# Performance work log

Hardware: AMD Instinct MI355X
Metric: run time of the kernel (lower is better)

Reference implementation:

```python
import jax, jax.numpy as jnp
import numpy as np

N, D, T = 4096, 256, 8
RHO = 16.0
DT = 1.0 / T


def setup_inputs() -> dict:
    key = jax.random.key(0)
    k1, k2, k3, k4 = jax.random.split(key, 4)
    X = jax.random.normal(k1, (N, D), dtype=jnp.float32)
    # learned deformation parameters (small init so the Euler flow stays stable)
    A = jax.random.normal(k2, (T, N, D), dtype=jnp.float32) * 0.01
    A_aff = jax.random.normal(k3, (T, D, D), dtype=jnp.float32) * 0.01
    b_aff = jax.random.normal(k4, (T, D), dtype=jnp.float32) * 0.01
    return {"X": X, "A": A, "A_aff": A_aff, "b_aff": b_aff}


def _flow(X, A, A_aff, b_aff):
    inv_two_rho2 = 1.0 / (2.0 * RHO * RHO)

    def step(Z, params_t):
        A_t, Aaff_t, baff_t = params_t
        # Gaussian self-kernel K[i,j] = exp(-||z_i - z_j||^2 / (2 rho^2))
        sq = jnp.sum(Z * Z, axis=1)                      # [n]
        dist = sq[:, None] + sq[None, :] - 2.0 * (Z @ Z.T)  # [n, n]
        K = jnp.exp(-dist * inv_two_rho2)
        # velocity: affine part + RKHS (kernel message aggregation) part
        v = Z @ Aaff_t.T + baff_t[None, :] + K @ A_t     # [n, d]
        return Z + DT * v, None

    Z_final, _ = jax.lax.scan(step, X, (A, A_aff, b_aff))
    return Z_final


def reference(X, A, A_aff, b_aff):
    return _flow(X, A, A_aff, b_aff)
```

## Files before the change

kernel.cpp:

```cpp
#include <hip/hip_runtime.h>


#define N_PTS 4096
#define DIM   256
#define DT_C  0.125f
#define C1    (1.0f/512.0f)

typedef __bf16 bf16x8 __attribute__((ext_vector_type(8)));
typedef float  f32x16 __attribute__((ext_vector_type(16)));
typedef float  f32x4v __attribute__((ext_vector_type(4)));
typedef unsigned int   u32x4 __attribute__((ext_vector_type(4)));
typedef unsigned short u16x8 __attribute__((ext_vector_type(8)));

__device__ __forceinline__ unsigned short f2bf(float f) {
  unsigned int u = __builtin_bit_cast(unsigned int, f);
  u += 0x7fffu + ((u >> 16) & 1u);
  return (unsigned short)(u >> 16);
}
__device__ __forceinline__ float bf2f(unsigned short s) {
  unsigned int u = ((unsigned int)s) << 16;
  return __builtin_bit_cast(float, u);
}

__global__ __launch_bounds__(256) void k_prep(const float* __restrict__ A,
                                              unsigned short* __restrict__ ATf) {
  __shared__ float sT[64][36];
  const int jgrp = blockIdx.x, ds = blockIdx.y, t = blockIdx.z;
  const int tid = threadIdx.x;
  const float* Ab = A + (size_t)t * N_PTS * DIM;
  {
    const int j_l = tid >> 2, dq = tid & 3;
    const float* src = Ab + (size_t)(jgrp * 64 + j_l) * DIM + ds * 32 + dq * 8;
    f32x4v v0 = *(const f32x4v*)src, v1 = *(const f32x4v*)(src + 4);
    *(f32x4v*)&sT[j_l][dq * 8] = v0;
    *(f32x4v*)&sT[j_l][dq * 8 + 4] = v1;
  }
  __syncthreads();
  const int jb_l = tid >> 6, l = tid & 63, l31 = l & 31, lhi = l >> 5;
  u16x8 o;
#pragma unroll
  for (int e = 0; e < 8; ++e) o[e] = f2bf(sT[jb_l * 16 + lhi * 8 + e][l31]);
  unsigned short* dst = ATf + (size_t)t * (8 * 256 * 64 * 8)
                      + ((size_t)(ds * 256 + jgrp * 4 + jb_l) * 64 + l) * 8;
  *(u16x8*)dst = o;
}

__global__ __launch_bounds__(256) void k_init(const float* __restrict__ X,
                                              unsigned short* __restrict__ Zf,
                                              float* __restrict__ erow) {
  const int tid = threadIdx.x;
  const int r = blockIdx.x * 8 + (tid >> 5), o = tid & 31;
  const size_t base = (size_t)r * DIM + o * 8;
  f32x4v z0 = *(const f32x4v*)(X + base), z1 = *(const f32x4v*)(X + base + 4);
  u16x8 zb; float s = 0.f;
#pragma unroll
  for (int i = 0; i < 4; ++i) { zb[i] = f2bf(z0[i]); zb[4 + i] = f2bf(z1[i]);
                                s += z0[i] * z0[i] + z1[i] * z1[i]; }
  *(u16x8*)(Zf + ((size_t)((r >> 5) * 16 + (o >> 1)) * 64 + (o & 1) * 32 + (r & 31)) * 8) = zb;
#pragma unroll
  for (int d = 16; d > 0; d >>= 1) s += __shfl_down(s, d, 32);
  if (o == 0) erow[r] = __expf(-s * C1);
}

__global__ __launch_bounds__(512, 4) void k_flash(
    const unsigned short* __restrict__ Zf, const float* __restrict__ erow,
    const unsigned short* __restrict__ ATf_t,
    const float* __restrict__ Aaff_t,
    unsigned short* __restrict__ Opart) {
  __shared__ unsigned short sP[2][64 * 64];

  const int tid = threadIdx.x, lane = tid & 63, wid = tid >> 6;
  const int l31 = lane & 31, lhi = lane >> 5;
  const int chunk = blockIdx.x;
  const int i0 = blockIdx.y * 64;
  const int ib = i0 >> 5;

  if (wid < 4) {
    const int ip = wid >> 1, jh = wid & 1;
    bf16x8 af[16];
    {
      const unsigned short* ap = Zf + ((size_t)(ib + ip) * 16 * 64 + lane) * 8;
#pragma unroll
      for (int ks = 0; ks < 16; ++ks)
        af[ks] = __builtin_bit_cast(bf16x8, *(const u32x4*)(ap + ks * 512));
    }
    float eI[16];
#pragma unroll
    for (int c = 0; c < 16; ++c)
      eI[c] = erow[i0 + ip * 32 + 4 * lhi + (c & 3) + 8 * (c >> 2)];

    for (int n = 0; n < 8; ++n) {
      f32x16 S;
#pragma unroll
      for (int i = 0; i < 16; ++i) S[i] = 0.f;
      {
        const int jblk = chunk * 16 + n * 2 + jh;
        const unsigned short* bp = Zf + ((size_t)jblk * 16 * 64 + lane) * 8;
#pragma unroll
        for (int ks = 0; ks < 16; ++ks) {
          bf16x8 b = __builtin_bit_cast(bf16x8, *(const u32x4*)(bp + ks * 512));
          S = __builtin_amdgcn_mfma_f32_32x32x16_bf16(af[ks], b, S, 0, 0, 0);
        }
      }
      const float ej = erow[chunk * 512 + n * 64 + jh * 32 + l31];
      unsigned short* pb = sP[n & 1];
      const int blk = jh * 4 + (l31 >> 3), cl = l31 & 7;
#pragma unroll
      for (int c = 0; c < 16; ++c) {
        const int row = ip * 32 + 4 * lhi + (c & 3) + 8 * (c >> 2);
        pb[row * 64 + ((blk ^ (row & 7)) * 8) + cl] =
            f2bf(eI[c] * ej * __expf(2.f * C1 * S[c]));
      }
      __syncthreads();
    }
    __syncthreads();
  } else {
    const int cd = wid - 4;
    f32x16 O[2][2];
#pragma unroll
    for (int rs = 0; rs < 2; ++rs)
#pragma unroll
      for (int ct = 0; ct < 2; ++ct)
#pragma unroll
        for (int i = 0; i < 16; ++i) O[rs][ct][i] = 0.f;

#pragma unroll
    for (int q = 0; q < 2; ++q) {
      const int ksg = chunk * 2 + q;
      bf16x8 a[2];
#pragma unroll
      for (int rs = 0; rs < 2; ++rs)
        a[rs] = __builtin_bit_cast(bf16x8, *(const u32x4*)(
            Zf + (((size_t)(ib + rs) * 16 + ksg) * 64 + lane) * 8));
#pragma unroll
      for (int ct = 0; ct < 2; ++ct) {
        const int d = cd * 64 + ct * 32 + l31;
        const float* bp = Aaff_t + (size_t)d * DIM + ksg * 16 + lhi * 8;
        f32x4v f0 = *(const f32x4v*)bp, f1 = *(const f32x4v*)(bp + 4);
        u16x8 tb;
#pragma unroll
        for (int i = 0; i < 4; ++i) { tb[i] = f2bf(f0[i]); tb[4 + i] = f2bf(f1[i]); }
        bf16x8 bv = __builtin_bit_cast(bf16x8, tb);
#pragma unroll
        for (int rs = 0; rs < 2; ++rs)
          O[rs][ct] = __builtin_amdgcn_mfma_f32_32x32x16_bf16(a[rs], bv, O[rs][ct], 0, 0, 0);
      }
    }
    __syncthreads();

    for (int n = 1; n <= 8; ++n) {
      const int m = n - 1;
      const unsigned short* pb = sP[m & 1];
#pragma unroll
      for (int ks = 0; ks < 4; ++ks) {
        bf16x8 a[2], b[2];
        const int blk = ks * 2 + lhi;
#pragma unroll
        for (int rs = 0; rs < 2; ++rs) {
          const int row = rs * 32 + l31;
          a[rs] = *(const bf16x8*)&pb[row * 64 + ((blk ^ (row & 7)) * 8)];
        }
#pragma unroll
        for (int ct = 0; ct < 2; ++ct)
          b[ct] = __builtin_bit_cast(bf16x8, *(const u32x4*)(ATf_t +
              ((size_t)((cd * 2 + ct) * 256 + chunk * 32 + m * 4 + ks) * 64 + lane) * 8));
#pragma unroll
        for (int rs = 0; rs < 2; ++rs)
#pragma unroll
          for (int ct = 0; ct < 2; ++ct)
            O[rs][ct] = __builtin_amdgcn_mfma_f32_32x32x16_bf16(a[rs], b[ct], O[rs][ct], 0, 0, 0);
      }
      __syncthreads();
    }

    unsigned short* ob = Opart + (size_t)chunk * N_PTS * DIM + (size_t)cd * 64 + l31;
#pragma unroll
    for (int rs = 0; rs < 2; ++rs)
#pragma unroll
      for (int c = 0; c < 16; ++c) {
        const int row = i0 + rs * 32 + 4 * lhi + (c & 3) + 8 * (c >> 2);
        ob[(size_t)row * DIM]      = f2bf(O[rs][0][c]);
        ob[(size_t)row * DIM + 32] = f2bf(O[rs][1][c]);
      }
  }
}

__global__ __launch_bounds__(256) void k_update(const float* __restrict__ Zin,
                                                const unsigned short* __restrict__ Opart,
                                                const float* __restrict__ baff_t,
                                                float* __restrict__ Zout,
                                                unsigned short* __restrict__ Zf,
                                                float* __restrict__ erow) {
  const int tid = threadIdx.x;
  const int r = blockIdx.x * 8 + (tid >> 5), o = tid & 31;
  const size_t base = (size_t)r * DIM + o * 8;
  f32x4v z0 = *(const f32x4v*)(Zin + base), z1 = *(const f32x4v*)(Zin + base + 4);
  f32x4v s0 = *(const f32x4v*)(baff_t + o * 8), s1 = *(const f32x4v*)(baff_t + o * 8 + 4);
#pragma unroll
  for (int c = 0; c < 8; ++c) {
    u16x8 p = *(const u16x8*)(Opart + (size_t)c * N_PTS * DIM + base);
#pragma unroll
    for (int i = 0; i < 4; ++i) { s0[i] += bf2f(p[i]); s1[i] += bf2f(p[4 + i]); }
  }
  u16x8 zb; float sv = 0.f;
#pragma unroll
  for (int i = 0; i < 4; ++i) {
    z0[i] += DT_C * s0[i]; z1[i] += DT_C * s1[i];
    zb[i] = f2bf(z0[i]); zb[4 + i] = f2bf(z1[i]);
    sv += z0[i] * z0[i] + z1[i] * z1[i];
  }
  *(f32x4v*)(Zout + base) = z0;
  *(f32x4v*)(Zout + base + 4) = z1;
  *(u16x8*)(Zf + ((size_t)((r >> 5) * 16 + (o >> 1)) * 64 + (o & 1) * 32 + (r & 31)) * 8) = zb;
#pragma unroll
  for (int d = 16; d > 0; d >>= 1) sv += __shfl_down(sv, d, 32);
  if (o == 0) erow[r] = __expf(-sv * C1);
}

extern "C" void kernel_launch(void* const* d_in, const int* in_sizes, int n_in,
                              void* d_out, int out_size, void* d_ws, size_t ws_size,
                              hipStream_t stream) {
  const float* X    = (const float*)d_in[0];
  const float* A    = (const float*)d_in[1];
  const float* Aaff = (const float*)d_in[2];
  const float* baff = (const float*)d_in[3];
  float* out = (float*)d_out;

  char* w = (char*)d_ws;
  size_t off = 0;
  unsigned short* ATf = (unsigned short*)(w + off); off += (size_t)8 * 8 * 256 * 64 * 8 * 2;
  unsigned short* Zf  = (unsigned short*)(w + off); off += (size_t)N_PTS * DIM * 2;
  float* erow = (float*)(w + off); off += (size_t)N_PTS * 4;
  float* Zf32 = (float*)(w + off); off += (size_t)N_PTS * DIM * 4;
  unsigned short* Opart = (unsigned short*)(w + off); off += (size_t)8 * N_PTS * DIM * 2;
  (void)ws_size; (void)in_sizes; (void)n_in; (void)out_size;

  k_prep<<<dim3(64, 8, 8), 256, 0, stream>>>(A, ATf);
  k_init<<<512, 256, 0, stream>>>(X, Zf, erow);

  const float* zin = X;
  for (int t = 0; t < 8; ++t) {
    float* zout = (t == 7) ? out : Zf32;
    k_flash<<<dim3(8, 64), 512, 0, stream>>>(
        Zf, erow, ATf + (size_t)t * (8 * 256 * 64 * 8), Aaff + (size_t)t * DIM * DIM, Opart);
    k_update<<<512, 256, 0, stream>>>(zin, Opart, baff + (size_t)t * DIM, zout, Zf, erow);
    zin = zout;
  }
}
```

Measured before the change: 391.3 us.

## Fuse score and aggregation per wave, keeping kernel tile in registers

Replaces the producer/consumer warp split in k_flash (4 waves computing exp scores into shared memory, 4 waves consuming them) with 4 waves that each compute scores via transposed MFMA and feed them directly as the B operand of the K@A MFMA, using lane shuffles instead of LDS and __syncthreads. Block size drops to 256 threads, register-prefetched Z_j and A tiles overlap with the math, and output is staged through a per-wave LDS bounce buffer for coalesced 16-byte stores. Each wave now recomputes its own score tile for its half of D, which doubles the score MFMA work, and register pressure rises.

```diff
diff --git a/kernel.cpp b/kernel.cpp
--- a/kernel.cpp
+++ b/kernel.cpp
@@ -20,6 +20,10 @@
 __device__ __forceinline__ float bf2f(unsigned short s) {
   unsigned int u = ((unsigned int)s) << 16;
   return __builtin_bit_cast(float, u);
+}
+__device__ __forceinline__ unsigned int packtr(float lo, float hi) {
+  return __builtin_amdgcn_perm(__builtin_bit_cast(unsigned int, hi),
+                               __builtin_bit_cast(unsigned int, lo), 0x07060302u);
 }
 
 __global__ __launch_bounds__(256) void k_prep(const float* __restrict__ A,
@@ -62,126 +66,157 @@
   if (o == 0) erow[r] = __expf(-s * C1);
 }
 
-__global__ __launch_bounds__(512, 4) void k_flash(
+__global__ __launch_bounds__(256, 2) void k_flash(
     const unsigned short* __restrict__ Zf, const float* __restrict__ erow,
     const unsigned short* __restrict__ ATf_t,
     const float* __restrict__ Aaff_t,
     unsigned short* __restrict__ Opart) {
-  __shared__ unsigned short sP[2][64 * 64];
+  __shared__ __align__(16) unsigned short bounce[4][32 * 136];
 
   const int tid = threadIdx.x, lane = tid & 63, wid = tid >> 6;
   const int l31 = lane & 31, lhi = lane >> 5;
+  const int isub = wid & 1, dh = wid >> 1;
   const int chunk = blockIdx.x;
   const int i0 = blockIdx.y * 64;
-  const int ib = i0 >> 5;
-
-  if (wid < 4) {
-    const int ip = wid >> 1, jh = wid & 1;
-    bf16x8 af[16];
+
+  bf16x8 zi[16];
+  {
+    const unsigned short* zp = Zf + ((size_t)(blockIdx.y * 2 + isub) * 16 * 64 + lane) * 8;
+#pragma unroll
+    for (int ks = 0; ks < 16; ++ks)
+      zi[ks] = __builtin_bit_cast(bf16x8, *(const u32x4*)(zp + ks * 512));
+  }
+  const float ei = erow[i0 + isub * 32 + l31];
+
+  f32x16 Op[4];
+#pragma unroll
+  for (int d = 0; d < 4; ++d)
+#pragma unroll
+    for (int i = 0; i < 16; ++i) Op[d][i] = 0.f;
+
+#pragma unroll
+  for (int q = 0; q < 2; ++q) {
+    const int ksg = chunk * 2 + q;
+    bf16x8 bzi = zi[ksg];
+#pragma unroll
+    for (int dblk = 0; dblk < 4; ++dblk) {
+      const int d = dh * 128 + dblk * 32 + l31;
+      const float* ap = Aaff_t + (size_t)d * DIM + ksg * 16 + lhi * 8;
+      f32x4v f0 = *(const f32x4v*)ap, f1 = *(const f32x4v*)(ap + 4);
+      u16x8 tb;
+#pragma unroll
+      for (int i = 0; i < 4; ++i) { tb[i] = f2bf(f0[i]); tb[4 + i] = f2bf(f1[i]); }
+      Op[dblk] = __builtin_amdgcn_mfma_f32_32x32x16_bf16(
+          __builtin_bit_cast(bf16x8, tb), bzi, Op[dblk], 0, 0, 0);
+    }
+  }
+
+  const unsigned short* zjbase = Zf + ((size_t)(chunk * 16) * 16 * 64 + lane) * 8;
+  const unsigned short* atbase = ATf_t + ((size_t)(dh * 4 * 256 + chunk * 32) * 64 + lane) * 8;
+  const float* ejbase = erow + chunk * 512 + 4 * lhi;
+
+  u32x4 zj[8], at[8];
+  u32x4 B0 = {0, 0, 0, 0}, B1 = {0, 0, 0, 0};
+#pragma unroll
+  for (int k = 0; k < 8; ++k) zj[k] = *(const u32x4*)(zjbase + (size_t)k * 512);
+
+#pragma unroll 1
+  for (int n = 0; n < 16; ++n) {
+    if (n) {
+      bf16x8 bb0 = __builtin_bit_cast(bf16x8, B0);
+      bf16x8 bb1 = __builtin_bit_cast(bf16x8, B1);
+#pragma unroll
+      for (int dblk = 0; dblk < 4; ++dblk)
+        Op[dblk] = __builtin_amdgcn_mfma_f32_32x32x16_bf16(
+            __builtin_bit_cast(bf16x8, at[dblk * 2]), bb0, Op[dblk], 0, 0, 0);
+#pragma unroll
+      for (int dblk = 0; dblk < 4; ++dblk)
+        Op[dblk] = __builtin_amdgcn_mfma_f32_32x32x16_bf16(
+            __builtin_bit_cast(bf16x8, at[dblk * 2 + 1]), bb1, Op[dblk], 0, 0, 0);
+    }
+#pragma unroll
+    for (int dblk = 0; dblk < 4; ++dblk)
+#pragma unroll
+      for (int s = 0; s < 2; ++s)
+        at[dblk * 2 + s] = *(const u32x4*)(atbase +
+            ((size_t)dblk * 256 + n * 2 + s) * 512);
+
+    f32x16 Sa, Sb;
+#pragma unroll
+    for (int i = 0; i < 16; ++i) { Sa[i] = 0.f; Sb[i] = 0.f; }
     {
-      const unsigned short* ap = Zf + ((size_t)(ib + ip) * 16 * 64 + lane) * 8;
-#pragma unroll
-      for (int ks = 0; ks < 16; ++ks)
-        af[ks] = __builtin_bit_cast(bf16x8, *(const u32x4*)(ap + ks * 512));
-    }
-    float eI[16];
-#pragma unroll
-    for (int c = 0; c < 16; ++c)
-      eI[c] = erow[i0 + ip * 32 + 4 * lhi + (c & 3) + 8 * (c >> 2)];
-
-    for (int n = 0; n < 8; ++n) {
-      f32x16 S;
-#pragma unroll
-      for (int i = 0; i < 16; ++i) S[i] = 0.f;
-      {
-        const int jblk = chunk * 16 + n * 2 + jh;
-        const unsigned short* bp = Zf + ((size_t)jblk * 16 * 64 + lane) * 8;
-#pragma unroll
-        for (int ks = 0; ks < 16; ++ks) {
-          bf16x8 b = __builtin_bit_cast(bf16x8, *(const u32x4*)(bp + ks * 512));
-          S = __builtin_amdgcn_mfma_f32_32x32x16_bf16(af[ks], b, S, 0, 0, 0);
+      const unsigned short* zt = zjbase + (size_t)n * 8192;
+#pragma unroll
+      for (int k = 0; k < 8; ++k)
+        Sa = __builtin_amdgcn_mfma_f32_32x32x16_bf16(
+            __builtin_bit_cast(bf16x8, zj[k]), zi[k], Sa, 0, 0, 0);
+#pragma unroll
+      for (int k = 0; k < 8; ++k) zj[k] = *(const u32x4*)(zt + (size_t)(8 + k) * 512);
+#pragma unroll
+      for (int k = 0; k < 8; ++k)
+        Sb = __builtin_amdgcn_mfma_f32_32x32x16_bf16(
+            __builtin_bit_cast(bf16x8, zj[k]), zi[k + 8], Sb, 0, 0, 0);
+      if (n < 15) {
+#pragma unroll
+        for (int k = 0; k < 8; ++k)
+          zj[k] = *(const u32x4*)(zt + (size_t)(16 + k) * 512);
+      }
+    }
+    {
+      unsigned int G[8];
+#pragma unroll
+      for (int g = 0; g < 4; ++g) {
+        f32x4v ejv = *(const f32x4v*)(ejbase + n * 32 + 8 * g);
+#pragma unroll
+        for (int p = 0; p < 2; ++p) {
+          const int c = g * 4 + p * 2;
+          float p0 = ei * ejv[p * 2]     * __expf(2.f * C1 * (Sa[c] + Sb[c]));
+          float p1 = ei * ejv[p * 2 + 1] * __expf(2.f * C1 * (Sa[c + 1] + Sb[c + 1]));
+          G[g * 2 + p] = packtr(p0, p1);
         }
       }
-      const float ej = erow[chunk * 512 + n * 64 + jh * 32 + l31];
-      unsigned short* pb = sP[n & 1];
-      const int blk = jh * 4 + (l31 >> 3), cl = l31 & 7;
-#pragma unroll
-      for (int c = 0; c < 16; ++c) {
-        const int row = ip * 32 + 4 * lhi + (c & 3) + 8 * (c >> 2);
-        pb[row * 64 + ((blk ^ (row & 7)) * 8) + cl] =
-            f2bf(eI[c] * ej * __expf(2.f * C1 * S[c]));
+      unsigned int Gp[8];
+#pragma unroll
+      for (int r = 0; r < 8; ++r) Gp[r] = __shfl_xor((int)G[r], 32);
+      B0[0] = lhi ? Gp[2] : G[0];  B0[1] = lhi ? Gp[3] : G[1];
+      B0[2] = lhi ? G[2] : Gp[0];  B0[3] = lhi ? G[3] : Gp[1];
+      B1[0] = lhi ? Gp[6] : G[4];  B1[1] = lhi ? Gp[7] : G[5];
+      B1[2] = lhi ? G[6] : Gp[4];  B1[3] = lhi ? G[7] : Gp[5];
+    }
+  }
+  {
+    bf16x8 bb0 = __builtin_bit_cast(bf16x8, B0);
+    bf16x8 bb1 = __builtin_bit_cast(bf16x8, B1);
+#pragma unroll
+    for (int dblk = 0; dblk < 4; ++dblk)
+      Op[dblk] = __builtin_amdgcn_mfma_f32_32x32x16_bf16(
+          __builtin_bit_cast(bf16x8, at[dblk * 2]), bb0, Op[dblk], 0, 0, 0);
+#pragma unroll
+    for (int dblk = 0; dblk < 4; ++dblk)
+      Op[dblk] = __builtin_amdgcn_mfma_f32_32x32x16_bf16(
+          __builtin_bit_cast(bf16x8, at[dblk * 2 + 1]), bb1, Op[dblk], 0, 0, 0);
+  }
+
+  {
+    unsigned short* bw = &bounce[wid][0];
+#pragma unroll
+    for (int dblk = 0; dblk < 4; ++dblk)
+#pragma unroll
+      for (int p = 0; p < 8; ++p) {
+        const int c = 2 * p;
+        const int dloc = dblk * 32 + 4 * lhi + (c & 3) + 8 * (c >> 2);
+        unsigned int v = (unsigned int)f2bf(Op[dblk][c]) |
+                         ((unsigned int)f2bf(Op[dblk][c + 1]) << 16);
+        *(unsigned int*)(bw + l31 * 136 + dloc) = v;
       }
-      __syncthreads();
-    }
-    __syncthreads();
-  } else {
-    const int cd = wid - 4;
-    f32x16 O[2][2];
-#pragma unroll
-    for (int rs = 0; rs < 2; ++rs)
-#pragma unroll
-      for (int ct = 0; ct < 2; ++ct)
-#pragma unroll
-        for (int i = 0; i < 16; ++i) O[rs][ct][i] = 0.f;
-
-#pragma unroll
-    for (int q = 0; q < 2; ++q) {
-      const int ksg = chunk * 2 + q;
-      bf16x8 a[2];
-#pragma unroll
-      for (int rs = 0; rs < 2; ++rs)
-        a[rs] = __builtin_bit_cast(bf16x8, *(const u32x4*)(
-            Zf + (((size_t)(ib + rs) * 16 + ksg) * 64 + lane) * 8));
-#pragma unroll
-      for (int ct = 0; ct < 2; ++ct) {
-        const int d = cd * 64 + ct * 32 + l31;
-        const float* bp = Aaff_t + (size_t)d * DIM + ksg * 16 + lhi * 8;
-        f32x4v f0 = *(const f32x4v*)bp, f1 = *(const f32x4v*)(bp + 4);
-        u16x8 tb;
-#pragma unroll
-        for (int i = 0; i < 4; ++i) { tb[i] = f2bf(f0[i]); tb[4 + i] = f2bf(f1[i]); }
-        bf16x8 bv = __builtin_bit_cast(bf16x8, tb);
-#pragma unroll
-        for (int rs = 0; rs < 2; ++rs)
-          O[rs][ct] = __builtin_amdgcn_mfma_f32_32x32x16_bf16(a[rs], bv, O[rs][ct], 0, 0, 0);
-      }
-    }
-    __syncthreads();
-
-    for (int n = 1; n <= 8; ++n) {
-      const int m = n - 1;
-      const unsigned short* pb = sP[m & 1];
-#pragma unroll
-      for (int ks = 0; ks < 4; ++ks) {
-        bf16x8 a[2], b[2];
-        const int blk = ks * 2 + lhi;
-#pragma unroll
-        for (int rs = 0; rs < 2; ++rs) {
-          const int row = rs * 32 + l31;
-          a[rs] = *(const bf16x8*)&pb[row * 64 + ((blk ^ (row & 7)) * 8)];
-        }
-#pragma unroll
-        for (int ct = 0; ct < 2; ++ct)
-          b[ct] = __builtin_bit_cast(bf16x8, *(const u32x4*)(ATf_t +
-              ((size_t)((cd * 2 + ct) * 256 + chunk * 32 + m * 4 + ks) * 64 + lane) * 8));
-#pragma unroll
-        for (int rs = 0; rs < 2; ++rs)
-#pragma unroll
-          for (int ct = 0; ct < 2; ++ct)
-            O[rs][ct] = __builtin_amdgcn_mfma_f32_32x32x16_bf16(a[rs], b[ct], O[rs][ct], 0, 0, 0);
-      }
-      __syncthreads();
-    }
-
-    unsigned short* ob = Opart + (size_t)chunk * N_PTS * DIM + (size_t)cd * 64 + l31;
-#pragma unroll
-    for (int rs = 0; rs < 2; ++rs)
-#pragma unroll
-      for (int c = 0; c < 16; ++c) {
-        const int row = i0 + rs * 32 + 4 * lhi + (c & 3) + 8 * (c >> 2);
-        ob[(size_t)row * DIM]      = f2bf(O[rs][0][c]);
-        ob[(size_t)row * DIM + 32] = f2bf(O[rs][1][c]);
-      }
+    unsigned short* ob = Opart + (size_t)chunk * N_PTS * DIM;
+#pragma unroll
+    for (int p = 0; p < 8; ++p) {
+      const int row = p * 4 + (lane >> 4);
+      const int col = (lane & 15) * 8;
+      u32x4 v = *(const u32x4*)(bw + row * 136 + col);
+      *(u32x4*)(ob + (size_t)(i0 + isub * 32 + row) * DIM + dh * 128 + col) = v;
+    }
   }
 }
 
@@ -241,7 +276,7 @@
   const float* zin = X;
   for (int t = 0; t < 8; ++t) {
     float* zout = (t == 7) ? out : Zf32;
-    k_flash<<<dim3(8, 64), 512, 0, stream>>>(
+    k_flash<<<dim3(8, 64), 256, 0, stream>>>(
         Zf, erow, ATf + (size_t)t * (8 * 256 * 64 * 8), Aaff + (size_t)t * DIM * DIM, Opart);
     k_update<<<512, 256, 0, stream>>>(zin, Opart, baff + (size_t)t * DIM, zout, Zf, erow);
     zin = zout;
```

Result: slower. 507.5 us (+29.7%).
